# Optimization experiments

Measured on AMD Instinct MI355X. Metric: run time of the kernel, lower is better.

The kernel has to match this reference:

```python
import jax, jax.numpy as jnp
import numpy as np

B, N, C, H, WS, SS = 16, 4096, 512, 8, 8, 4
HD = C // H
SCALE = HD ** -0.5
NW = N // WS  # number of mask windows (= 512)
B_ = B * NW   # windows-times-batch after the view(-1, WS, C)


def _make_mask():
    # faithful replication of create_mask(), including the non-standard
    # window_partition (reshape->transpose->reshape) used by the repo
    img = np.zeros(N, dtype=np.float32)
    img[N - WS:N - SS] = 1.0
    img[N - SS:] = 2.0
    # window_partition on (1, N, 1) then .view(-1, WS):
    mw = img.reshape(N // WS, WS).T.reshape(N // WS, WS)  # (NW, WS)
    am = mw[:, None, :] - mw[:, :, None]                   # (NW, WS, WS)
    return jnp.asarray(np.where(am != 0.0, -100.0, 0.0).astype(np.float32))

ATTN_MASK = _make_mask()  # (NW, WS, WS)


def _layernorm(x, w, b, eps=1e-5):
    mu = jnp.mean(x, axis=-1, keepdims=True)
    var = jnp.mean((x - mu) ** 2, axis=-1, keepdims=True)
    return (x - mu) * jax.lax.rsqrt(var + eps) * w + b


def setup_inputs() -> dict:
    key = jax.random.key(0)
    ks = jax.random.split(key, 8)
    s = 0.02
    return {
        'x': jax.random.normal(ks[0], (B, N, C), jnp.float32),
        'norm1_w': jnp.ones((C,), jnp.float32),
        'norm1_b': jnp.zeros((C,), jnp.float32),
        'qkv_w': jax.random.normal(ks[1], (C, 3 * C), jnp.float32) * s,
        'qkv_b': jnp.zeros((3 * C,), jnp.float32),
        'proj_w': jax.random.normal(ks[2], (C, C), jnp.float32) * s,
        'proj_b': jnp.zeros((C,), jnp.float32),
        'norm2_w': jnp.ones((C,), jnp.float32),
        'norm2_b': jnp.zeros((C,), jnp.float32),
        'mlp_w1': jax.random.normal(ks[3], (C, 4 * C), jnp.float32) * s,
        'mlp_b1': jnp.zeros((4 * C,), jnp.float32),
        'mlp_w2': jax.random.normal(ks[4], (4 * C, C), jnp.float32) * s,
        'mlp_b2': jnp.zeros((C,), jnp.float32),
    }


def reference(x, norm1_w, norm1_b, qkv_w, qkv_b, proj_w, proj_b,
              norm2_w, norm2_b, mlp_w1, mlp_b1, mlp_w2, mlp_b2):
    shortcut = x
    h = _layernorm(x, norm1_w, norm1_b)
    h = jnp.roll(h, -SS, axis=1)  # shift_size > 0
    # repo's window_partition: (B,N,C) -> (B, N//WS, WS, C) -> perm -> (B*WS, N//WS, C)
    win = h.reshape(B, N // WS, WS, C).transpose(0, 2, 1, 3)
    # then .view(-1, WS, C): reinterpret flat buffer as (B_, WS, C)
    win = win.reshape(B_, WS, C)
    qkv = (win @ qkv_w + qkv_b).reshape(B_, WS, 3, H, HD).transpose(2, 0, 3, 1, 4)
    q, k, v = qkv[0], qkv[1], qkv[2]              # (B_, H, WS, HD)
    attn = jnp.einsum('bhqd,bhkd->bhqk', q, k) * SCALE
    attn = attn.reshape(B, NW, H, WS, WS) + ATTN_MASK[None, :, None]
    attn = jax.nn.softmax(attn.reshape(B_, H, WS, WS), axis=-1)
    out = jnp.einsum('bhqk,bhkd->bqhd', attn, v).reshape(B_, WS, C)
    out = out @ proj_w + proj_b
    # repo's window_reverse on the (B_, WS, C) buffer
    out = out.reshape(B, N // WS, WS, C).transpose(0, 2, 1, 3).reshape(B, N, C)
    out = jnp.roll(out, SS, axis=1)
    x = shortcut + out
    h2 = _layernorm(x, norm2_w, norm2_b)
    h2 = jax.nn.gelu(h2 @ mlp_w1 + mlp_b1, approximate=False)
    return x + (h2 @ mlp_w2 + mlp_b2)
```

## Files before the change

kernel.cpp:

```cpp
#include <hip/hip_runtime.h>
#include <hip/hip_bf16.h>
#include <cstdint>
#include <cstddef>

typedef __hip_bfloat16 BF16;
typedef __bf16 bf16x8 __attribute__((ext_vector_type(8)));
typedef float floatx4 __attribute__((ext_vector_type(4)));

static constexpr size_t OFF_WQKV  = 0;
static constexpr size_t OFF_WPROJ = OFF_WQKV  + (size_t)1536 * 512 * 2;
static constexpr size_t OFF_W1    = OFF_WPROJ + (size_t)512 * 512 * 2;
static constexpr size_t OFF_W2    = OFF_W1    + (size_t)2048 * 512 * 2;
static constexpr size_t OFF_H     = OFF_W2    + (size_t)512 * 2048 * 2;
static constexpr size_t OFF_QKV   = OFF_H     + (size_t)65536 * 512 * 2;
static constexpr size_t OFF_ATTN  = OFF_QKV   + (size_t)65536 * 1536 * 2;
static constexpr size_t OFF_M     = OFF_QKV;

__global__ __launch_bounds__(256) void wprep_kernel(
    const float* __restrict__ W, BF16* __restrict__ Wt, int K, int N) {
  __shared__ float t[64][65];
  const int n0 = blockIdx.x * 64, k0 = blockIdx.y * 64;
  const int tid = threadIdx.x;
#pragma unroll
  for (int it = 0; it < 16; ++it) {
    int idx = it * 256 + tid;
    int r = idx >> 6, c = idx & 63;
    t[r][c] = W[(size_t)(k0 + r) * N + (n0 + c)];
  }
  __syncthreads();
#pragma unroll
  for (int it = 0; it < 16; ++it) {
    int idx = it * 256 + tid;
    int r = idx >> 6, c = idx & 63;
    Wt[(size_t)(n0 + r) * K + (k0 + c)] = __float2bfloat16(t[c][r]);
  }
}

__global__ __launch_bounds__(256) void ln_kernel(
    const float* __restrict__ x, const float* __restrict__ w,
    const float* __restrict__ b, BF16* __restrict__ out) {
  const int lane = threadIdx.x & 63;
  const size_t row = (size_t)blockIdx.x * 4 + (threadIdx.x >> 6);
  const float* xr = x + row * 512 + lane * 8;
  float xv[8], wv[8], bv[8];
  *(float4*)&xv[0] = *(const float4*)xr;
  *(float4*)&xv[4] = *(const float4*)(xr + 4);
  *(float4*)&wv[0] = *(const float4*)(w + lane * 8);
  *(float4*)&wv[4] = *(const float4*)(w + lane * 8 + 4);
  *(float4*)&bv[0] = *(const float4*)(b + lane * 8);
  *(float4*)&bv[4] = *(const float4*)(b + lane * 8 + 4);
  float s = 0.0f, ss = 0.0f;
#pragma unroll
  for (int t = 0; t < 8; ++t) { s += xv[t]; ss += xv[t] * xv[t]; }
#pragma unroll
  for (int o = 32; o > 0; o >>= 1) { s += __shfl_xor(s, o); ss += __shfl_xor(ss, o); }
  const float mu = s * (1.0f / 512.0f);
  const float var = ss * (1.0f / 512.0f) - mu * mu;
  const float rs = rsqrtf(var + 1e-5f);
  BF16 ob[8];
#pragma unroll
  for (int t = 0; t < 8; ++t)
    ob[t] = __float2bfloat16((xv[t] - mu) * rs * wv[t] + bv[t]);
  *(uint4*)(out + row * 512 + lane * 8) = *(const uint4*)ob;
}

__device__ __forceinline__ void gload16(const BF16* g, const char* l) {
  __builtin_amdgcn_global_load_lds(
      (const __attribute__((address_space(1))) void*)g,
      (__attribute__((address_space(3))) void*)l, 16, 0, 0);
}

__device__ __forceinline__ int win_src_row(int r) {
  const int b = r >> 12;
  const int s = (r >> 9) & 7;
  const int mm = (r >> 3) & 63;
  const int j = r & 7;
  const int p = (64 * mm + 8 * j + s + 4) & 4095;
  return (b << 12) + p;
}

__device__ __forceinline__ float fast_gelu(float v) {
  const float x = fabsf(v) * 0.70710678118654752f;
  const float t = __builtin_amdgcn_rcpf(1.0f + 0.3275911f * x);
  const float poly = t * (0.254829592f +
                     t * (-0.284496736f +
                     t * (1.421413741f +
                     t * (-1.453152027f +
                     t * 1.061405429f))));
  const float erfc_ = poly * __expf(-x * x);
  const float erfv = copysignf(1.0f - erfc_, v);
  return 0.5f * v * (1.0f + erfv);
}

#define GATE8 asm volatile("s_waitcnt vmcnt(8)" ::: "memory")
#define GATE0 asm volatile("s_waitcnt vmcnt(0)" ::: "memory")
#define BAR() __builtin_amdgcn_s_barrier()
#define WAITL() asm volatile("s_waitcnt lgkmcnt(0)" ::: "memory")

template <int ROWMAP, int EPI, int K>
__global__ __launch_bounds__(256, 2) void gemm128(
    const BF16* __restrict__ A, const BF16* __restrict__ Bt,
    const float* __restrict__ bias, const float* __restrict__ resid,
    float* __restrict__ outf, BF16* __restrict__ outb, int Nout) {
  __shared__ __align__(16) char smem[65536];
  const int tid = threadIdx.x, lane = tid & 63, wv = tid >> 6;
  const int wm = wv >> 1, wn = wv & 1;

  const int gx = gridDim.x;
  const int nwg = gx * gridDim.y;
  const int hwid = blockIdx.y * gx + blockIdx.x;
  const int swz = (hwid & 7) * (nwg >> 3) + (hwid >> 3);
  const int bm = swz / gx, bn = swz - bm * gx;
  const int row0 = bm * 128, col0 = bn * 128;

  const int srow = lane >> 3;
  const int scol = ((lane & 7) ^ srow) * 8;
  const BF16* Pa[4];
  const BF16* Pb[4];
#pragma unroll
  for (int c = 0; c < 4; ++c) {
    int ra = row0 + c * 32 + wv * 8 + srow;
    if (ROWMAP == 1) ra = win_src_row(ra);
    Pa[c] = A + (size_t)ra * K + scol;
    const int rb = col0 + c * 32 + wv * 8 + srow;
    Pb[c] = Bt + (size_t)rb * K + scol;
  }

  const int r16 = lane & 15;
  const int sx0 = (((lane >> 4) + 0) ^ (r16 & 7)) * 16;
  const int sx1 = (((lane >> 4) + 4) ^ (r16 & 7)) * 16;
  const int raby = (wm * 64 + r16) * 128;
  const int rbby = 32768 + (wn * 64 + r16) * 128;

  floatx4 acc[4][4];
#pragma unroll
  for (int m = 0; m < 4; ++m)
#pragma unroll
    for (int n = 0; n < 4; ++n) acc[m][n] = floatx4{0.f, 0.f, 0.f, 0.f};

  bf16x8 fa[4][2], fb[4][2];

#define STG(dd) do {                                                   \
    _Pragma("unroll")                                                  \
    for (int c = 0; c < 4; ++c)                                        \
      gload16(Pa[c], smem + (dd)*16384 + c*4096 + wv*1024);            \
    _Pragma("unroll")                                                  \
    for (int c = 0; c < 4; ++c)                                        \
      gload16(Pb[c], smem + 32768 + (dd)*16384 + c*4096 + wv*1024);    \
    _Pragma("unroll")                                                  \
    for (int c = 0; c < 4; ++c) { Pa[c] += 64; Pb[c] += 64; }          \
  } while (0)

#define RDS(dd) do {                                                          \
    _Pragma("unroll")                                                         \
    for (int m = 0; m < 4; ++m) {                                             \
      fa[m][0] = *(const bf16x8*)(smem + (dd)*16384 + raby + m*2048 + sx0);   \
      fa[m][1] = *(const bf16x8*)(smem + (dd)*16384 + raby + m*2048 + sx1);   \
    }                                                                         \
    _Pragma("unroll")                                                         \
    for (int n = 0; n < 4; ++n) {                                             \
      fb[n][0] = *(const bf16x8*)(smem + (dd)*16384 + rbby + n*2048 + sx0);   \
      fb[n][1] = *(const bf16x8*)(smem + (dd)*16384 + rbby + n*2048 + sx1);   \
    }                                                                         \
  } while (0)

#define MF() do {                                                             \
    __builtin_amdgcn_s_setprio(1);                                            \
    _Pragma("unroll")                                                         \
    for (int ks = 0; ks < 2; ++ks)                                            \
      _Pragma("unroll")                                                       \
      for (int m = 0; m < 4; ++m)                                             \
        _Pragma("unroll")                                                     \
        for (int n = 0; n < 4; ++n)                                           \
          acc[m][n] = __builtin_amdgcn_mfma_f32_16x16x32_bf16(                \
              fa[m][ks], fb[n][ks], acc[m][n], 0, 0, 0);                      \
    __builtin_amdgcn_s_setprio(0);                                            \
  } while (0)

  constexpr int NT = K / 64;
  STG(0);
  for (int t = 0; t < NT - 1; ++t) {
    const int dd = t & 1, de = dd ^ 1;
    STG(de);
    GATE8;
    BAR();
    RDS(dd);
    WAITL();
    MF();
    BAR();
  }
  {
    const int dd = (NT - 1) & 1;
    GATE0;
    BAR();
    RDS(dd);
    WAITL();
    MF();
  }
#undef STG
#undef RDS
#undef MF

  float bsv[4];
#pragma unroll
  for (int n = 0; n < 4; ++n) bsv[n] = bias[col0 + wn * 64 + n * 16 + r16];

#pragma unroll
  for (int m = 0; m < 4; ++m) {
    const int rbase = row0 + wm * 64 + m * 16 + (lane >> 4) * 4;
#pragma unroll
    for (int n = 0; n < 4; ++n) {
      const int col = col0 + wn * 64 + n * 16 + r16;
#pragma unroll
      for (int e = 0; e < 4; ++e) {
        const int r = rbase + e;
        float v = acc[m][n][e] + bsv[n];
        if (EPI == 0) {
          outb[(size_t)r * Nout + col] = __float2bfloat16(v);
        } else if (EPI == 1) {
          outb[(size_t)r * Nout + col] = __float2bfloat16(fast_gelu(v));
        } else if (EPI == 2) {
          const int b = r >> 12;
          const int np = (r >> 3) & 511;
          const int ap = r & 7;
          const int io = ((ap << 9) + np + 4) & 4095;
          const size_t o = ((size_t)(b << 12) + io) * 512 + col;
          outf[o] = resid[o] + v;
        } else {
          const size_t o = (size_t)r * 512 + col;
          outf[o] += v;
        }
      }
    }
  }
}

__global__ __launch_bounds__(64) void attn_kernel(
    const BF16* __restrict__ qkv, BF16* __restrict__ out) {
  const int w = blockIdx.x;
  const int lane = threadIdx.x;
  const int qi = lane >> 3, kj = lane & 7;
  __shared__ __align__(16) BF16 sm[8 * 1544];
  const BF16* src = qkv + (size_t)w * 8 * 1536;
#pragma unroll
  for (int rr = 0; rr < 8; ++rr) {
    const uint4* s4 = (const uint4*)(src + (size_t)rr * 1536);
    uint4* d4 = (uint4*)(&sm[rr * 1544]);
#pragma unroll
    for (int c = 0; c < 3; ++c) d4[c * 64 + lane] = s4[c * 64 + lane];
  }
  __syncthreads();

  const int s = (w >> 6) & 7, mm = w & 63;
  const int pi = 64 * mm + 8 * qi + s;
  const int pj = 64 * mm + 8 * kj + s;
  const int ri = pi >= 4092 ? 2 : (pi >= 4088 ? 1 : 0);
  const int rj = pj >= 4092 ? 2 : (pj >= 4088 ? 1 : 0);
  const float maskv = (ri != rj) ? -100.0f : 0.0f;

  for (int h = 0; h < 8; ++h) {
    const BF16* qp = &sm[qi * 1544 + h * 64];
    const BF16* kp = &sm[kj * 1544 + 512 + h * 64];
    float acc = 0.0f;
#pragma unroll
    for (int d0 = 0; d0 < 8; ++d0) {
      bf16x8 qv = *(const bf16x8*)(qp + d0 * 8);
      bf16x8 kv = *(const bf16x8*)(kp + d0 * 8);
#pragma unroll
      for (int t = 0; t < 8; ++t) acc += (float)qv[t] * (float)kv[t];
    }
    float sc = acc * 0.125f + maskv;
    float mx = sc;
    mx = fmaxf(mx, __shfl_xor(mx, 1, 8));
    mx = fmaxf(mx, __shfl_xor(mx, 2, 8));
    mx = fmaxf(mx, __shfl_xor(mx, 4, 8));
    float e = __expf(sc - mx);
    float den = e;
    den += __shfl_xor(den, 1, 8);
    den += __shfl_xor(den, 2, 8);
    den += __shfl_xor(den, 4, 8);
    const float P = e / den;

    float o8[8];
#pragma unroll
    for (int t = 0; t < 8; ++t) o8[t] = 0.0f;
#pragma unroll
    for (int j2 = 0; j2 < 8; ++j2) {
      float p2 = __shfl(P, j2, 8);
      bf16x8 vv = *(const bf16x8*)(&sm[j2 * 1544 + 1024 + h * 64 + kj * 8]);
#pragma unroll
      for (int t = 0; t < 8; ++t) o8[t] += p2 * (float)vv[t];
    }
    BF16 ob[8];
#pragma unroll
    for (int t = 0; t < 8; ++t) ob[t] = __float2bfloat16(o8[t]);
    *(uint4*)(&out[((size_t)w * 8 + qi) * 512 + h * 64 + kj * 8]) = *(const uint4*)ob;
  }
}

extern "C" void kernel_launch(void* const* d_in, const int* in_sizes, int n_in,
                              void* d_out, int out_size, void* d_ws, size_t ws_size,
                              hipStream_t stream) {
  (void)in_sizes; (void)n_in; (void)out_size; (void)ws_size;
  const float* x     = (const float*)d_in[0];
  const float* n1w   = (const float*)d_in[1];
  const float* n1b   = (const float*)d_in[2];
  const float* qkvw  = (const float*)d_in[3];
  const float* qkvb  = (const float*)d_in[4];
  const float* projw = (const float*)d_in[5];
  const float* projb = (const float*)d_in[6];
  const float* n2w   = (const float*)d_in[7];
  const float* n2b   = (const float*)d_in[8];
  const float* w1    = (const float*)d_in[9];
  const float* b1    = (const float*)d_in[10];
  const float* w2    = (const float*)d_in[11];
  const float* b2    = (const float*)d_in[12];
  float* out = (float*)d_out;
  char* ws = (char*)d_ws;

  BF16* wt_qkv  = (BF16*)(ws + OFF_WQKV);
  BF16* wt_proj = (BF16*)(ws + OFF_WPROJ);
  BF16* wt_w1   = (BF16*)(ws + OFF_W1);
  BF16* wt_w2   = (BF16*)(ws + OFF_W2);
  BF16* hbuf    = (BF16*)(ws + OFF_H);
  BF16* qkvbuf  = (BF16*)(ws + OFF_QKV);
  BF16* attnbuf = (BF16*)(ws + OFF_ATTN);
  BF16* mbuf    = (BF16*)(ws + OFF_M);

  wprep_kernel<<<dim3(24, 8), 256, 0, stream>>>(qkvw, wt_qkv, 512, 1536);
  wprep_kernel<<<dim3(8, 8), 256, 0, stream>>>(projw, wt_proj, 512, 512);
  wprep_kernel<<<dim3(32, 8), 256, 0, stream>>>(w1, wt_w1, 512, 2048);
  wprep_kernel<<<dim3(8, 32), 256, 0, stream>>>(w2, wt_w2, 2048, 512);

  ln_kernel<<<16384, 256, 0, stream>>>(x, n1w, n1b, hbuf);
  gemm128<1, 0, 512><<<dim3(12, 512), 256, 0, stream>>>(hbuf, wt_qkv, qkvb, nullptr, nullptr, qkvbuf, 1536);
  attn_kernel<<<8192, 64, 0, stream>>>(qkvbuf, attnbuf);
  gemm128<0, 2, 512><<<dim3(4, 512), 256, 0, stream>>>(attnbuf, wt_proj, projb, x, out, nullptr, 512);
  ln_kernel<<<16384, 256, 0, stream>>>(out, n2w, n2b, hbuf);
  gemm128<0, 1, 512><<<dim3(16, 512), 256, 0, stream>>>(hbuf, wt_w1, b1, nullptr, nullptr, mbuf, 2048);
  gemm128<0, 3, 2048><<<dim3(4, 512), 256, 0, stream>>>(mbuf, wt_w2, b2, nullptr, out, nullptr, 512);
}
```

Measured before the change: 758.7 us.

## Make GEMM blocks persistent over four M tiles with a continuous prefetch pipeline

Each GEMM workgroup now handles four consecutive 128-row tiles rather than one, and the next tile's first K-slab is prefetched while the current tile's last slab is computed. The grid shrinks fourfold, so launch and pipeline-fill costs are spread over more work. The trade-off is fewer workgroups (about 1536 to 8192 down to 384 to 2048 per GEMM), which could hurt load balance and latency hiding on a part with many CUs. The epilogue also runs inside the loop, so the barriers and the pipeline stall there.

```diff
diff --git a/kernel.cpp b/kernel.cpp
--- a/kernel.cpp
+++ b/kernel.cpp
@@ -97,7 +97,7 @@
 #define BAR() __builtin_amdgcn_s_barrier()
 #define WAITL() asm volatile("s_waitcnt lgkmcnt(0)" ::: "memory")
 
-template <int ROWMAP, int EPI, int K>
+template <int ROWMAP, int EPI, int K, int MT>
 __global__ __launch_bounds__(256, 2) void gemm128(
     const BF16* __restrict__ A, const BF16* __restrict__ Bt,
     const float* __restrict__ bias, const float* __restrict__ resid,
@@ -111,7 +111,7 @@
   const int hwid = blockIdx.y * gx + blockIdx.x;
   const int swz = (hwid & 7) * (nwg >> 3) + (hwid >> 3);
   const int bm = swz / gx, bn = swz - bm * gx;
-  const int row0 = bm * 128, col0 = bn * 128;
+  const int row00 = bm * 128 * MT, col0 = bn * 128;
 
   const int srow = lane >> 3;
   const int scol = ((lane & 7) ^ srow) * 8;
@@ -119,7 +119,7 @@
   const BF16* Pb[4];
 #pragma unroll
   for (int c = 0; c < 4; ++c) {
-    int ra = row0 + c * 32 + wv * 8 + srow;
+    int ra = row00 + c * 32 + wv * 8 + srow;
     if (ROWMAP == 1) ra = win_src_row(ra);
     Pa[c] = A + (size_t)ra * K + scol;
     const int rb = col0 + c * 32 + wv * 8 + srow;
@@ -179,60 +179,84 @@
 
   constexpr int NT = K / 64;
   STG(0);
-  for (int t = 0; t < NT - 1; ++t) {
-    const int dd = t & 1, de = dd ^ 1;
-    STG(de);
-    GATE8;
-    BAR();
-    RDS(dd);
-    WAITL();
-    MF();
-    BAR();
-  }
-  {
-    const int dd = (NT - 1) & 1;
-    GATE0;
-    BAR();
-    RDS(dd);
-    WAITL();
-    MF();
+  int p = 0;
+  int row0m = row00;
+
+  for (int mt = 0; mt < MT; ++mt) {
+    for (int t = 0; t < NT; ++t) {
+      const int dd = p & 1, de = dd ^ 1;
+      const bool lastg = (mt == MT - 1) && (t == NT - 1);
+      if (t == NT - 1 && !lastg) {
+        if (ROWMAP == 1) {
+#pragma unroll
+          for (int c = 0; c < 4; ++c) {
+            int ra = row0m + 128 + c * 32 + wv * 8 + srow;
+            ra = win_src_row(ra);
+            Pa[c] = A + (size_t)ra * K + scol;
+          }
+        } else {
+#pragma unroll
+          for (int c = 0; c < 4; ++c) Pa[c] += (size_t)127 * K;
+        }
+#pragma unroll
+        for (int c = 0; c < 4; ++c) Pb[c] -= K;
+      }
+      if (!lastg) {
+        STG(de);
+        GATE8;
+      } else {
+        GATE0;
+      }
+      BAR();
+      RDS(dd);
+      WAITL();
+      MF();
+      BAR();
+      ++p;
+    }
+
+    {
+      float bsv[4];
+#pragma unroll
+      for (int n = 0; n < 4; ++n) bsv[n] = bias[col0 + wn * 64 + n * 16 + r16];
+#pragma unroll
+      for (int m = 0; m < 4; ++m) {
+        const int rbase = row0m + wm * 64 + m * 16 + (lane >> 4) * 4;
+#pragma unroll
+        for (int n = 0; n < 4; ++n) {
+          const int col = col0 + wn * 64 + n * 16 + r16;
+#pragma unroll
+          for (int e = 0; e < 4; ++e) {
+            const int r = rbase + e;
+            float v = acc[m][n][e] + bsv[n];
+            if (EPI == 0) {
+              outb[(size_t)r * Nout + col] = __float2bfloat16(v);
+            } else if (EPI == 1) {
+              outb[(size_t)r * Nout + col] = __float2bfloat16(fast_gelu(v));
+            } else if (EPI == 2) {
+              const int b = r >> 12;
+              const int np = (r >> 3) & 511;
+              const int ap = r & 7;
+              const int io = ((ap << 9) + np + 4) & 4095;
+              const size_t o = ((size_t)(b << 12) + io) * 512 + col;
+              outf[o] = resid[o] + v;
+            } else {
+              const size_t o = (size_t)r * 512 + col;
+              outf[o] += v;
+            }
+          }
+        }
+      }
+#pragma unroll
+      for (int m = 0; m < 4; ++m)
+#pragma unroll
+        for (int n = 0; n < 4; ++n) acc[m][n] = floatx4{0.f, 0.f, 0.f, 0.f};
+    }
+    row0m += 128;
   }
 #undef STG
 #undef RDS
 #undef MF
-
-  float bsv[4];
-#pragma unroll
-  for (int n = 0; n < 4; ++n) bsv[n] = bias[col0 + wn * 64 + n * 16 + r16];
-
-#pragma unroll
-  for (int m = 0; m < 4; ++m) {
-    const int rbase = row0 + wm * 64 + m * 16 + (lane >> 4) * 4;
-#pragma unroll
-    for (int n = 0; n < 4; ++n) {
-      const int col = col0 + wn * 64 + n * 16 + r16;
-#pragma unroll
-      for (int e = 0; e < 4; ++e) {
-        const int r = rbase + e;
-        float v = acc[m][n][e] + bsv[n];
-        if (EPI == 0) {
-          outb[(size_t)r * Nout + col] = __float2bfloat16(v);
-        } else if (EPI == 1) {
-          outb[(size_t)r * Nout + col] = __float2bfloat16(fast_gelu(v));
-        } else if (EPI == 2) {
-          const int b = r >> 12;
-          const int np = (r >> 3) & 511;
-          const int ap = r & 7;
-          const int io = ((ap << 9) + np + 4) & 4095;
-          const size_t o = ((size_t)(b << 12) + io) * 512 + col;
-          outf[o] = resid[o] + v;
-        } else {
-          const size_t o = (size_t)r * 512 + col;
-          outf[o] += v;
-        }
-      }
-    }
-  }
 }
 
 __global__ __launch_bounds__(64) void attn_kernel(
@@ -333,10 +357,10 @@
   wprep_kernel<<<dim3(8, 32), 256, 0, stream>>>(w2, wt_w2, 2048, 512);
 
   ln_kernel<<<16384, 256, 0, stream>>>(x, n1w, n1b, hbuf);
-  gemm128<1, 0, 512><<<dim3(12, 512), 256, 0, stream>>>(hbuf, wt_qkv, qkvb, nullptr, nullptr, qkvbuf, 1536);
+  gemm128<1, 0, 512, 4><<<dim3(12, 128), 256, 0, stream>>>(hbuf, wt_qkv, qkvb, nullptr, nullptr, qkvbuf, 1536);
   attn_kernel<<<8192, 64, 0, stream>>>(qkvbuf, attnbuf);
-  gemm128<0, 2, 512><<<dim3(4, 512), 256, 0, stream>>>(attnbuf, wt_proj, projb, x, out, nullptr, 512);
+  gemm128<0, 2, 512, 4><<<dim3(4, 128), 256, 0, stream>>>(attnbuf, wt_proj, projb, x, out, nullptr, 512);
   ln_kernel<<<16384, 256, 0, stream>>>(out, n2w, n2b, hbuf);
-  gemm128<0, 1, 512><<<dim3(16, 512), 256, 0, stream>>>(hbuf, wt_w1, b1, nullptr, nullptr, mbuf, 2048);
-  gemm128<0, 3, 2048><<<dim3(4, 512), 256, 0, stream>>>(mbuf, wt_w2, b2, nullptr, out, nullptr, 512);
-}
+  gemm128<0, 1, 512, 4><<<dim3(16, 128), 256, 0, stream>>>(hbuf, wt_w1, b1, nullptr, nullptr, mbuf, 2048);
+  gemm128<0, 3, 2048, 4><<<dim3(4, 128), 256, 0, stream>>>(mbuf, wt_w2, b2, nullptr, out, nullptr, 512);
+}
```

Measured after the change: 779.8 us. 2.8% more time.

## Use 8-wave GEMM blocks, vectorized epilogue, and sigmoid-based GELU

Applied to the files above, without the earlier changes.

Each GEMM workgroup grows from 4 to 8 waves, and each wave now owns a 32x64 sub-tile, which halves per-wave accumulator and fragment registers so more waves fit per CU. The MFMA operands are swapped so each lane holds four consecutive output columns. That lets the epilogue issue vectorized bias loads, packed bf16 stores and float4 residual read-modify-writes instead of scalar accesses. The erf-based GELU is replaced by the cheaper x*sigmoid(1.702x) approximation, which changes numerics and risks accuracy against the exact reference. Explicit LDS waits are dropped and the vmcnt gate is lowered to match the smaller per-thread load count.

```diff
diff --git a/kernel.cpp b/kernel.cpp
--- a/kernel.cpp
+++ b/kernel.cpp
@@ -80,25 +80,23 @@
 }
 
 __device__ __forceinline__ float fast_gelu(float v) {
-  const float x = fabsf(v) * 0.70710678118654752f;
-  const float t = __builtin_amdgcn_rcpf(1.0f + 0.3275911f * x);
-  const float poly = t * (0.254829592f +
-                     t * (-0.284496736f +
-                     t * (1.421413741f +
-                     t * (-1.453152027f +
-                     t * 1.061405429f))));
-  const float erfc_ = poly * __expf(-x * x);
-  const float erfv = copysignf(1.0f - erfc_, v);
-  return 0.5f * v * (1.0f + erfv);
-}
-
-#define GATE8 asm volatile("s_waitcnt vmcnt(8)" ::: "memory")
+  const float t = __expf(v * -1.702f);
+  return v * __builtin_amdgcn_rcpf(1.0f + t);
+}
+
+__device__ __forceinline__ uint2 pack4bf(float a, float b, float c, float d) {
+  union { BF16 h[4]; uint2 u; } u;
+  u.h[0] = __float2bfloat16(a); u.h[1] = __float2bfloat16(b);
+  u.h[2] = __float2bfloat16(c); u.h[3] = __float2bfloat16(d);
+  return u.u;
+}
+
+#define GATE4 asm volatile("s_waitcnt vmcnt(4)" ::: "memory")
 #define GATE0 asm volatile("s_waitcnt vmcnt(0)" ::: "memory")
 #define BAR() __builtin_amdgcn_s_barrier()
-#define WAITL() asm volatile("s_waitcnt lgkmcnt(0)" ::: "memory")
 
 template <int ROWMAP, int EPI, int K>
-__global__ __launch_bounds__(256, 2) void gemm128(
+__global__ __launch_bounds__(512, 4) void gemm128(
     const BF16* __restrict__ A, const BF16* __restrict__ Bt,
     const float* __restrict__ bias, const float* __restrict__ resid,
     float* __restrict__ outf, BF16* __restrict__ outb, int Nout) {
@@ -115,66 +113,62 @@
 
   const int srow = lane >> 3;
   const int scol = ((lane & 7) ^ srow) * 8;
-  const BF16* Pa[4];
-  const BF16* Pb[4];
-#pragma unroll
-  for (int c = 0; c < 4; ++c) {
-    int ra = row0 + c * 32 + wv * 8 + srow;
-    if (ROWMAP == 1) ra = win_src_row(ra);
-    Pa[c] = A + (size_t)ra * K + scol;
-    const int rb = col0 + c * 32 + wv * 8 + srow;
-    Pb[c] = Bt + (size_t)rb * K + scol;
-  }
+  int ra0 = row0 + wv * 16 + srow;
+  int ra1 = row0 + wv * 16 + 8 + srow;
+  if (ROWMAP == 1) { ra0 = win_src_row(ra0); ra1 = win_src_row(ra1); }
+  const BF16* Pa0 = A + (size_t)ra0 * K + scol;
+  const BF16* Pa1 = A + (size_t)ra1 * K + scol;
+  const BF16* Pb0 = Bt + (size_t)(col0 + wv * 16 + srow) * K + scol;
+  const BF16* Pb1 = Bt + (size_t)(col0 + wv * 16 + 8 + srow) * K + scol;
+  const int ldsw = wv * 2048;
 
   const int r16 = lane & 15;
-  const int sx0 = (((lane >> 4) + 0) ^ (r16 & 7)) * 16;
-  const int sx1 = (((lane >> 4) + 4) ^ (r16 & 7)) * 16;
-  const int raby = (wm * 64 + r16) * 128;
+  const int g = lane >> 4;
+  const int sx0 = ((g + 0) ^ (r16 & 7)) * 16;
+  const int sx1 = ((g + 4) ^ (r16 & 7)) * 16;
+  const int raby = (wm * 32 + r16) * 128;
   const int rbby = 32768 + (wn * 64 + r16) * 128;
 
-  floatx4 acc[4][4];
-#pragma unroll
-  for (int m = 0; m < 4; ++m)
-#pragma unroll
-    for (int n = 0; n < 4; ++n) acc[m][n] = floatx4{0.f, 0.f, 0.f, 0.f};
-
-  bf16x8 fa[4][2], fb[4][2];
-
-#define STG(dd) do {                                                   \
-    _Pragma("unroll")                                                  \
-    for (int c = 0; c < 4; ++c)                                        \
-      gload16(Pa[c], smem + (dd)*16384 + c*4096 + wv*1024);            \
-    _Pragma("unroll")                                                  \
-    for (int c = 0; c < 4; ++c)                                        \
-      gload16(Pb[c], smem + 32768 + (dd)*16384 + c*4096 + wv*1024);    \
-    _Pragma("unroll")                                                  \
-    for (int c = 0; c < 4; ++c) { Pa[c] += 64; Pb[c] += 64; }          \
+  floatx4 acc[2][4];
+#pragma unroll
+  for (int m2 = 0; m2 < 2; ++m2)
+#pragma unroll
+    for (int n2 = 0; n2 < 4; ++n2) acc[m2][n2] = floatx4{0.f, 0.f, 0.f, 0.f};
+
+  bf16x8 fa[2][2], fb[4][2];
+
+#define STG(dd) do {                                          \
+    gload16(Pa0, smem + (dd)*16384 + ldsw);                   \
+    gload16(Pa1, smem + (dd)*16384 + ldsw + 1024);            \
+    gload16(Pb0, smem + 32768 + (dd)*16384 + ldsw);           \
+    gload16(Pb1, smem + 32768 + (dd)*16384 + ldsw + 1024);    \
+    Pa0 += 64; Pa1 += 64; Pb0 += 64; Pb1 += 64;               \
   } while (0)
 
-#define RDS(dd) do {                                                          \
-    _Pragma("unroll")                                                         \
-    for (int m = 0; m < 4; ++m) {                                             \
-      fa[m][0] = *(const bf16x8*)(smem + (dd)*16384 + raby + m*2048 + sx0);   \
-      fa[m][1] = *(const bf16x8*)(smem + (dd)*16384 + raby + m*2048 + sx1);   \
-    }                                                                         \
-    _Pragma("unroll")                                                         \
-    for (int n = 0; n < 4; ++n) {                                             \
-      fb[n][0] = *(const bf16x8*)(smem + (dd)*16384 + rbby + n*2048 + sx0);   \
-      fb[n][1] = *(const bf16x8*)(smem + (dd)*16384 + rbby + n*2048 + sx1);   \
-    }                                                                         \
+#define RDS(dd) do {                                                           \
+    _Pragma("unroll")                                                          \
+    for (int m2 = 0; m2 < 2; ++m2) {                                           \
+      fa[m2][0] = *(const bf16x8*)(smem + (dd)*16384 + raby + m2*2048 + sx0);  \
+      fa[m2][1] = *(const bf16x8*)(smem + (dd)*16384 + raby + m2*2048 + sx1);  \
+    }                                                                          \
+    _Pragma("unroll")                                                          \
+    for (int n2 = 0; n2 < 4; ++n2) {                                           \
+      fb[n2][0] = *(const bf16x8*)(smem + (dd)*16384 + rbby + n2*2048 + sx0);  \
+      fb[n2][1] = *(const bf16x8*)(smem + (dd)*16384 + rbby + n2*2048 + sx1);  \
+    }                                                                          \
   } while (0)
 
-#define MF() do {                                                             \
-    __builtin_amdgcn_s_setprio(1);                                            \
-    _Pragma("unroll")                                                         \
-    for (int ks = 0; ks < 2; ++ks)                                            \
-      _Pragma("unroll")                                                       \
-      for (int m = 0; m < 4; ++m)                                             \
-        _Pragma("unroll")                                                     \
-        for (int n = 0; n < 4; ++n)                                           \
-          acc[m][n] = __builtin_amdgcn_mfma_f32_16x16x32_bf16(                \
-              fa[m][ks], fb[n][ks], acc[m][n], 0, 0, 0);                      \
-    __builtin_amdgcn_s_setprio(0);                                            \
+#define MF() do {                                                              \
+    __builtin_amdgcn_s_setprio(1);                                             \
+    _Pragma("unroll")                                                          \
+    for (int ks = 0; ks < 2; ++ks)                                             \
+      _Pragma("unroll")                                                        \
+      for (int m2 = 0; m2 < 2; ++m2)                                           \
+        _Pragma("unroll")                                                      \
+        for (int n2 = 0; n2 < 4; ++n2)                                         \
+          acc[m2][n2] = __builtin_amdgcn_mfma_f32_16x16x32_bf16(               \
+              fb[n2][ks], fa[m2][ks], acc[m2][n2], 0, 0, 0);                   \
+    __builtin_amdgcn_s_setprio(0);                                             \
   } while (0)
 
   constexpr int NT = K / 64;
@@ -182,10 +176,9 @@
   for (int t = 0; t < NT - 1; ++t) {
     const int dd = t & 1, de = dd ^ 1;
     STG(de);
-    GATE8;
+    GATE4;
     BAR();
     RDS(dd);
-    WAITL();
     MF();
     BAR();
   }
@@ -194,42 +187,50 @@
     GATE0;
     BAR();
     RDS(dd);
-    WAITL();
     MF();
   }
 #undef STG
 #undef RDS
 #undef MF
 
-  float bsv[4];
-#pragma unroll
-  for (int n = 0; n < 4; ++n) bsv[n] = bias[col0 + wn * 64 + n * 16 + r16];
-
-#pragma unroll
-  for (int m = 0; m < 4; ++m) {
-    const int rbase = row0 + wm * 64 + m * 16 + (lane >> 4) * 4;
-#pragma unroll
-    for (int n = 0; n < 4; ++n) {
-      const int col = col0 + wn * 64 + n * 16 + r16;
-#pragma unroll
-      for (int e = 0; e < 4; ++e) {
-        const int r = rbase + e;
-        float v = acc[m][n][e] + bsv[n];
-        if (EPI == 0) {
-          outb[(size_t)r * Nout + col] = __float2bfloat16(v);
-        } else if (EPI == 1) {
-          outb[(size_t)r * Nout + col] = __float2bfloat16(fast_gelu(v));
-        } else if (EPI == 2) {
-          const int b = r >> 12;
-          const int np = (r >> 3) & 511;
-          const int ap = r & 7;
-          const int io = ((ap << 9) + np + 4) & 4095;
-          const size_t o = ((size_t)(b << 12) + io) * 512 + col;
-          outf[o] = resid[o] + v;
-        } else {
-          const size_t o = (size_t)r * 512 + col;
-          outf[o] += v;
-        }
+  const int g4 = g * 4;
+  float4 bsv[4];
+#pragma unroll
+  for (int n2 = 0; n2 < 4; ++n2)
+    bsv[n2] = *(const float4*)&bias[col0 + wn * 64 + n2 * 16 + g4];
+
+#pragma unroll
+  for (int m2 = 0; m2 < 2; ++m2) {
+    const int r = row0 + wm * 32 + m2 * 16 + r16;
+    size_t rowbase;
+    if (EPI == 2) {
+      const int b = r >> 12;
+      const int np = (r >> 3) & 511;
+      const int ap = r & 7;
+      const int io = ((ap << 9) + np + 4) & 4095;
+      rowbase = ((size_t)(b << 12) + io) * 512;
+    } else {
+      rowbase = (size_t)r * Nout;
+    }
+#pragma unroll
+    for (int n2 = 0; n2 < 4; ++n2) {
+      const int c0 = col0 + wn * 64 + n2 * 16 + g4;
+      floatx4 v = acc[m2][n2];
+      v[0] += bsv[n2].x; v[1] += bsv[n2].y;
+      v[2] += bsv[n2].z; v[3] += bsv[n2].w;
+      if (EPI == 0) {
+        *(uint2*)&outb[rowbase + c0] = pack4bf(v[0], v[1], v[2], v[3]);
+      } else if (EPI == 1) {
+        *(uint2*)&outb[rowbase + c0] = pack4bf(
+            fast_gelu(v[0]), fast_gelu(v[1]), fast_gelu(v[2]), fast_gelu(v[3]));
+      } else if (EPI == 2) {
+        const float4 rv = *(const float4*)&resid[rowbase + c0];
+        float4 ov = {rv.x + v[0], rv.y + v[1], rv.z + v[2], rv.w + v[3]};
+        *(float4*)&outf[rowbase + c0] = ov;
+      } else {
+        float4 ov = *(float4*)&outf[rowbase + c0];
+        ov.x += v[0]; ov.y += v[1]; ov.z += v[2]; ov.w += v[3];
+        *(float4*)&outf[rowbase + c0] = ov;
       }
     }
   }
@@ -333,10 +334,10 @@
   wprep_kernel<<<dim3(8, 32), 256, 0, stream>>>(w2, wt_w2, 2048, 512);
 
   ln_kernel<<<16384, 256, 0, stream>>>(x, n1w, n1b, hbuf);
-  gemm128<1, 0, 512><<<dim3(12, 512), 256, 0, stream>>>(hbuf, wt_qkv, qkvb, nullptr, nullptr, qkvbuf, 1536);
+  gemm128<1, 0, 512><<<dim3(12, 512), 512, 0, stream>>>(hbuf, wt_qkv, qkvb, nullptr, nullptr, qkvbuf, 1536);
   attn_kernel<<<8192, 64, 0, stream>>>(qkvbuf, attnbuf);
-  gemm128<0, 2, 512><<<dim3(4, 512), 256, 0, stream>>>(attnbuf, wt_proj, projb, x, out, nullptr, 512);
+  gemm128<0, 2, 512><<<dim3(4, 512), 512, 0, stream>>>(attnbuf, wt_proj, projb, x, out, nullptr, 512);
   ln_kernel<<<16384, 256, 0, stream>>>(out, n2w, n2b, hbuf);
-  gemm128<0, 1, 512><<<dim3(16, 512), 256, 0, stream>>>(hbuf, wt_w1, b1, nullptr, nullptr, mbuf, 2048);
-  gemm128<0, 3, 2048><<<dim3(4, 512), 256, 0, stream>>>(mbuf, wt_w2, b2, nullptr, out, nullptr, 512);
-}
+  gemm128<0, 1, 512><<<dim3(16, 512), 512, 0, stream>>>(hbuf, wt_w1, b1, nullptr, nullptr, mbuf, 2048);
+  gemm128<0, 3, 2048><<<dim3(4, 512), 512, 0, stream>>>(mbuf, wt_w2, b2, nullptr, out, nullptr, 512);
+}
```

Result: slower. 781.5 us (+3.0%).
